# Kernel optimization log

Hardware: AMD Instinct MI355X
Metric: run time of the kernel (lower is better)

Reference implementation:

```python
import jax, jax.numpy as jnp
import numpy as np

K = 3
STRIDE = 1
PAD = 1


def _conv2d(x, w, b):
    y = jax.lax.conv_general_dilated(
        x, w, window_strides=(STRIDE, STRIDE),
        padding=[(PAD, PAD), (PAD, PAD)],
        dimension_numbers=("NCHW", "OIHW", "NCHW"))
    return y + b[None, :, None, None]


def _bilinear_sample(xb, py, px):
    # xb: [C, H, W]; py, px: [K2, Ho, Wo] float sample coords
    C, H, W = xb.shape
    y0 = jnp.floor(py)
    x0 = jnp.floor(px)
    ay = py - y0  # frac weights
    ax = px - x0
    out = jnp.zeros((C,) + py.shape, dtype=xb.dtype)
    corners = [
        (y0, x0, (1.0 - ay) * (1.0 - ax)),
        (y0, x0 + 1.0, (1.0 - ay) * ax),
        (y0 + 1.0, x0, ay * (1.0 - ax)),
        (y0 + 1.0, x0 + 1.0, ay * ax),
    ]
    for yc, xc, wgt in corners:
        valid = (yc >= 0) & (yc < H) & (xc >= 0) & (xc < W)
        yi = jnp.clip(yc, 0, H - 1).astype(jnp.int32)
        xi = jnp.clip(xc, 0, W - 1).astype(jnp.int32)
        g = xb[:, yi, xi]  # [C, K2, Ho, Wo]
        out = out + g * (wgt * valid.astype(xb.dtype))[None]
    return out


def _deform_forward(x, weight, bias, p_weight, p_bias):
    B, Cin, H, W = x.shape
    Cout = weight.shape[0]
    K2 = K * K
    # offset / mask prediction conv
    pout = _conv2d(x, p_weight, p_bias)  # [B, 3*K2, Ho, Wo]
    o1, o2, m = jnp.split(pout, 3, axis=1)
    offset = jnp.concatenate([o1, o2], axis=1)  # [B, 2*K2, Ho, Wo]
    mask = jax.nn.sigmoid(m)  # [B, K2, Ho, Wo]
    Ho, Wo = mask.shape[2], mask.shape[3]
    # torchvision layout: channel 2k = dy_k, 2k+1 = dx_k
    off = offset.reshape(B, K2, 2, Ho, Wo)
    dy, dx = off[:, :, 0], off[:, :, 1]  # [B, K2, Ho, Wo]
    ki = (jnp.arange(K2) // K).astype(x.dtype)  # kernel row
    kj = (jnp.arange(K2) % K).astype(x.dtype)   # kernel col
    base_y = jnp.arange(Ho, dtype=x.dtype) * STRIDE - PAD  # [Ho]
    base_x = jnp.arange(Wo, dtype=x.dtype) * STRIDE - PAD  # [Wo]
    py = base_y[None, None, :, None] + ki[None, :, None, None] + dy
    px = base_x[None, None, None, :] + kj[None, :, None, None] + dx
    sampled = jax.vmap(_bilinear_sample)(x, py, px)  # [B, Cin, K2, Ho, Wo]
    sampled = sampled * mask[:, None]
    w = weight.reshape(Cout, Cin, K2)
    out = jnp.einsum('bckhw,ock->bohw', sampled, w) + bias[None, :, None, None]
    return out


def setup_inputs() -> dict:
    key = jax.random.key(0)
    k1, k2, k3 = jax.random.split(key, 3)
    B, Cin, Cout, H, W = 4, 256, 256, 64, 64
    x = jax.random.normal(k1, (B, Cin, H, W), dtype=jnp.float32)
    fan_in = Cin * K * K
    weight = jax.random.normal(k2, (Cout, Cin, K, K), dtype=jnp.float32) / np.sqrt(fan_in)
    bias = jnp.zeros((Cout,), dtype=jnp.float32)
    # small random offset/mask predictor (zero-init in the original; randomized
    # here so the deformable sampling path is exercised)
    p_weight = jax.random.normal(k3, (3 * K * K, Cin, K, K), dtype=jnp.float32) * 0.02
    p_bias = jnp.zeros((3 * K * K,), dtype=jnp.float32)
    return {"x": x, "weight": weight, "bias": bias, "p_weight": p_weight, "p_bias": p_bias}


def reference(x, weight, bias, p_weight, p_bias):
    return _deform_forward(x, weight, bias, p_weight, p_bias)
```

## Files before the change

kernel.cpp:

```cpp
#include <hip/hip_runtime.h>
#include <stdint.h>


#define CIN 256
#define COUT 256
#define HWS 4096
#define MTOT 16384
#define KTOT 2304
#define SPLITK 8

typedef __attribute__((ext_vector_type(8))) short bf16x8;
typedef __attribute__((ext_vector_type(4))) float f32x4;

__device__ __forceinline__ unsigned short f2bf(float f) {
  unsigned int u = __float_as_uint(f);
  unsigned int r = (u + 0x7fffu + ((u >> 16) & 1u)) >> 16;
  return (unsigned short)r;
}
__device__ __forceinline__ float bf2f(unsigned short u) {
  return __uint_as_float(((unsigned int)u) << 16);
}

__device__ __forceinline__ void gload_lds16(const void* g, void* l) {
  __builtin_amdgcn_global_load_lds((const __attribute__((address_space(1))) void*)g,
                                   (__attribute__((address_space(3))) void*)l, 16, 0, 0);
}

__global__ __launch_bounds__(256) void prep_and_transpose(const float* __restrict__ x,
                                                          const float* __restrict__ w,
                                                          const float* __restrict__ pw,
                                                          unsigned short* __restrict__ xt,
                                                          unsigned short* __restrict__ WB,
                                                          unsigned short* __restrict__ PWs,
                                                          unsigned short* __restrict__ zerop) {
  __shared__ float tile[32][33];
  int bid = blockIdx.x;
  if (bid < 4096) {
    int b = bid >> 10;
    int rest = bid & 1023;
    int hw0 = (rest & 127) * 32;
    int c0 = ((rest >> 7) & 7) * 32;
    int tx = threadIdx.x & 31, ty = threadIdx.x >> 5;
    for (int i = ty; i < 32; i += 8)
      tile[i][tx] = x[(size_t)(b * CIN + c0 + i) * HWS + hw0 + tx];
    __syncthreads();
    for (int r = ty; r < 32; r += 8)
      xt[(size_t)(b * HWS + hw0 + r) * CIN + c0 + tx] = f2bf(tile[tx][r]);
  } else {
    int idx = (bid - 4096) * 256 + threadIdx.x;
    if (idx < 512)
      *(uint4*)(zerop + idx * 8) = make_uint4(0, 0, 0, 0);
    if (idx < KTOT * COUT) {
      int f = idx;
      int e = f & 7;
      int row = (f >> 3) & 15;
      int quad = (f >> 7) & 3;
      int j = (f >> 9) & 15;
      int t = f >> 13;
      int kk = t * 32 + quad * 8 + e;
      int o = j * 16 + row;
      int k = kk >> 8, c = kk & 255;
      WB[f] = f2bf(w[o * KTOT + c * 9 + k]);
    } else {
      int f2 = idx - KTOT * COUT;
      int t_ = f2 & 7;
      int rest = f2 >> 3;
      int j = rest & 31;
      int kk = (rest >> 5) * 8 + t_;
      int k = kk >> 8, c = kk & 255;
      float v = (j < 27) ? pw[j * KTOT + c * 9 + k] : 0.0f;
      PWs[f2] = f2bf(v);
    }
  }
}

__global__ __launch_bounds__(256) void offset_conv_sk(const unsigned short* __restrict__ xt,
                                                      const unsigned short* __restrict__ PWs,
                                                      const unsigned short* __restrict__ zerop,
                                                      float* __restrict__ Pbuf) {
  __shared__ unsigned short Al[64 * 32];
  __shared__ unsigned short Bl[1024];
  int tid = threadIdx.x;
  int lane = tid & 63, wv = tid >> 6;
  int mt = (blockIdx.x & 7) * 32 + (blockIdx.x >> 3);
  int m0 = mt * 64;
  int s = blockIdx.y;
  int b = m0 >> 12;
  int hw0 = m0 & 4095;
  f32x4 acc[2] = {};

  for (int tt = 0; tt < 72 / SPLITK; ++tt) {
    int t = s * (72 / SPLITK) + tt;
    int k = t >> 3, c0 = (t & 7) * 32;
    int dyk = k / 3 - 1;
    int dxk = k % 3 - 1;
    __syncthreads();
    if (tid < 128)
      gload_lds16(PWs + (size_t)t * 1024 + tid * 8, &Bl[tid * 8]);
    {
      int r = tid >> 2;
      int hw = hw0 + r;
      int h = hw >> 6, wwp = hw & 63;
      int y = h + dyk, xx = wwp + dxk;
      bool valid = ((unsigned)y < 64u) && ((unsigned)xx < 64u);
      const unsigned short* src = valid
          ? xt + ((size_t)((b << 12) + (y << 6) + xx) << 8) + c0 + (tid & 3) * 8
          : zerop;
      gload_lds16(src, &Al[tid * 8]);
    }
    __syncthreads();
    int row = lane & 15, quad = lane >> 4;
    bf16x8 af = *(const bf16x8*)&Al[(wv * 16 + row) * 32 + quad * 8];
    for (int j = 0; j < 2; ++j) {
      bf16x8 bfr = *(const bf16x8*)&Bl[(quad * 32 + j * 16 + row) * 8];
      acc[j] = __builtin_amdgcn_mfma_f32_16x16x32_bf16(af, bfr, acc[j], 0, 0, 0);
    }
  }

  int row = lane & 15, quad = lane >> 4;
  for (int j = 0; j < 2; ++j) {
    int n = j * 16 + row;
    for (int r_ = 0; r_ < 4; ++r_) {
      int m = m0 + wv * 16 + quad * 4 + r_;
      Pbuf[((size_t)s * MTOT + m) * 32 + n] = acc[j][r_];
    }
  }
}

__global__ __launch_bounds__(256) void index_prep(const float* __restrict__ Pbuf,
                                                  const float* __restrict__ p_bias,
                                                  int4* __restrict__ DIW) {
  int gid = blockIdx.x * 256 + threadIdx.x;
  int m = gid / 9;
  int k = gid - m * 9;

  float dy = p_bias[2 * k];
  float dx = p_bias[2 * k + 1];
  float mv = p_bias[18 + k];
#pragma unroll
  for (int s = 0; s < SPLITK; ++s) {
    const float* p = Pbuf + ((size_t)s * MTOT + m) * 32;
    dy += p[2 * k];
    dx += p[2 * k + 1];
    mv += p[18 + k];
  }
  float mk = 1.0f / (1.0f + __expf(-mv));

  int hw = m & 4095, h = hw >> 6, ww = hw & 63;
  float py = (float)(h - 1 + k / 3) + dy;
  float px = (float)(ww - 1 + k % 3) + dx;
  float y0f = floorf(py), x0f = floorf(px);
  float ay = py - y0f, ax = px - x0f;
  int y0 = (int)y0f, x0 = (int)x0f;

  float w00 = (1.f - ay) * (1.f - ax) * mk;
  float w01 = (1.f - ay) * ax * mk;
  float w10 = ay * (1.f - ax) * mk;
  float w11 = ay * ax * mk;

  float vy0 = ((unsigned)y0 < 64u) ? 1.f : 0.f;
  float vy1 = ((unsigned)(y0 + 1) < 64u) ? 1.f : 0.f;
  float vx0 = ((unsigned)x0 < 64u) ? 1.f : 0.f;
  float vx1 = ((unsigned)(x0 + 1) < 64u) ? 1.f : 0.f;
  w00 *= vy0 * vx0; w01 *= vy0 * vx1; w10 *= vy1 * vx0; w11 *= vy1 * vx1;

  int yc0 = min(max(y0, 0), 63), yc1 = min(max(y0 + 1, 0), 63);
  int xc0 = min(max(x0, 0), 63), xc1 = min(max(x0 + 1, 0), 63);

  DIW[(size_t)gid * 2] = make_int4((yc0 * 64 + xc0) * 256, (yc0 * 64 + xc1) * 256,
                                   (yc1 * 64 + xc0) * 256, (yc1 * 64 + xc1) * 256);
  float4 w4 = make_float4(w00, w01, w10, w11);
  ((float4*)DIW)[(size_t)gid * 2 + 1] = w4;
}

__device__ __forceinline__ void bilin8(const bf16x8 g00, const bf16x8 g01,
                                       const bf16x8 g10, const bf16x8 g11,
                                       const float4 w4, unsigned short* dst) {
  bf16x8 o8;
#pragma unroll
  for (int e = 0; e < 8; ++e) {
    float v = w4.x * bf2f((unsigned short)g00[e]) + w4.y * bf2f((unsigned short)g01[e]) +
              w4.z * bf2f((unsigned short)g10[e]) + w4.w * bf2f((unsigned short)g11[e]);
    o8[e] = (short)f2bf(v);
  }
  *(bf16x8*)dst = o8;
}

#define MFMA16(A0, A1, A2_, A3, B0, B1, B2, B3)                                          \
  acc[0][0] = __builtin_amdgcn_mfma_f32_16x16x32_bf16(A0, B0, acc[0][0], 0, 0, 0);       \
  acc[0][1] = __builtin_amdgcn_mfma_f32_16x16x32_bf16(A0, B1, acc[0][1], 0, 0, 0);       \
  acc[0][2] = __builtin_amdgcn_mfma_f32_16x16x32_bf16(A0, B2, acc[0][2], 0, 0, 0);       \
  acc[0][3] = __builtin_amdgcn_mfma_f32_16x16x32_bf16(A0, B3, acc[0][3], 0, 0, 0);       \
  acc[1][0] = __builtin_amdgcn_mfma_f32_16x16x32_bf16(A1, B0, acc[1][0], 0, 0, 0);       \
  acc[1][1] = __builtin_amdgcn_mfma_f32_16x16x32_bf16(A1, B1, acc[1][1], 0, 0, 0);       \
  acc[1][2] = __builtin_amdgcn_mfma_f32_16x16x32_bf16(A1, B2, acc[1][2], 0, 0, 0);       \
  acc[1][3] = __builtin_amdgcn_mfma_f32_16x16x32_bf16(A1, B3, acc[1][3], 0, 0, 0);       \
  acc[2][0] = __builtin_amdgcn_mfma_f32_16x16x32_bf16(A2_, B0, acc[2][0], 0, 0, 0);      \
  acc[2][1] = __builtin_amdgcn_mfma_f32_16x16x32_bf16(A2_, B1, acc[2][1], 0, 0, 0);      \
  acc[2][2] = __builtin_amdgcn_mfma_f32_16x16x32_bf16(A2_, B2, acc[2][2], 0, 0, 0);      \
  acc[2][3] = __builtin_amdgcn_mfma_f32_16x16x32_bf16(A2_, B3, acc[2][3], 0, 0, 0);      \
  acc[3][0] = __builtin_amdgcn_mfma_f32_16x16x32_bf16(A3, B0, acc[3][0], 0, 0, 0);       \
  acc[3][1] = __builtin_amdgcn_mfma_f32_16x16x32_bf16(A3, B1, acc[3][1], 0, 0, 0);       \
  acc[3][2] = __builtin_amdgcn_mfma_f32_16x16x32_bf16(A3, B2, acc[3][2], 0, 0, 0);       \
  acc[3][3] = __builtin_amdgcn_mfma_f32_16x16x32_bf16(A3, B3, acc[3][3], 0, 0, 0);

#define FITER(T, PAR, BC0, BC1, BC2, BC3, BN0, BN1, BN2, BN3)                            \
  {                                                                                      \
    if ((T) <= 69) {                                                                     \
      if ((((T) + 2) & 7) == 0) dI4 = Tbl[r][((T) + 2) >> 3][0];                         \
      int cq = (((T) + 2) & 7) * 32 + qo;                                                \
      g00 = *(const bf16x8*)(xtb + dI4.x + cq);                                          \
      g01 = *(const bf16x8*)(xtb + dI4.y + cq);                                          \
      g10 = *(const bf16x8*)(xtb + dI4.z + cq);                                          \
      g11 = *(const bf16x8*)(xtb + dI4.w + cq);                                          \
    }                                                                                    \
    if ((T) <= 70) {                                                                     \
      const unsigned short* bt_ = bpb + (size_t)((T) + 1) * 8192;                        \
      BN0 = *(const bf16x8*)(bt_);                                                       \
      BN1 = *(const bf16x8*)(bt_ + 512);                                                 \
      BN2 = *(const bf16x8*)(bt_ + 1024);                                                \
      BN3 = *(const bf16x8*)(bt_ + 1536);                                                \
    }                                                                                    \
    afr0 = *(const bf16x8*)&As[PAR][row][quad * 8];                                      \
    afr1 = *(const bf16x8*)&As[PAR][16 + row][quad * 8];                                 \
    afr2 = *(const bf16x8*)&As[PAR][32 + row][quad * 8];                                 \
    afr3 = *(const bf16x8*)&As[PAR][48 + row][quad * 8];                                 \
    if ((T) <= 70) {                                                                     \
      if ((((T) + 1) & 7) == 0) dW4 = *(float4*)&Tbl[r][((T) + 1) >> 3][1];              \
      bilin8(gp0, gp1, gp2, gp3, dW4, &As[PAR ^ 1][r][qo]);                              \
    }                                                                                    \
    MFMA16(afr0, afr1, afr2, afr3, BC0, BC1, BC2, BC3)                                   \
    __syncthreads();                                                                     \
  }

__global__ __launch_bounds__(256, 1) void fused_gemm(const unsigned short* __restrict__ xt,
                                                     const int4* __restrict__ DIW,
                                                     const unsigned short* __restrict__ WB,
                                                     const float* __restrict__ bias,
                                                     float* __restrict__ out) {
  __shared__ unsigned short As[2][64][40];
  __shared__ int4 Tbl[64][9][2];

  int tid = threadIdx.x;
  int lane = tid & 63, wv = tid >> 6;
  int mt = (blockIdx.x & 7) * 32 + (blockIdx.x >> 3);
  int mb = mt * 64;
  int b = mb >> 12;
  int hw0 = mb & 4095;
  const unsigned short* xtb = xt + ((size_t)b << 20);

  {
    const int4* src = DIW + (size_t)mb * 18;
    int4* dst = (int4*)Tbl;
    for (int i = tid; i < 1152; i += 256)
      gload_lds16(src + i, dst + i);
  }
  __syncthreads();

  int r = tid >> 2;
  int qo = (tid & 3) * 8;

  int4 dI4 = Tbl[r][0][0];
  float4 dW4 = *(float4*)&Tbl[r][0][1];

  int row = lane & 15, quad = lane >> 4;
  const unsigned short* bpb = WB + (size_t)wv * 4 * 512 + quad * 128 + row * 8;

  f32x4 acc[4][4] = {};
  bf16x8 g00, g01, g10, g11;
  bf16x8 gp0, gp1, gp2, gp3;
  bf16x8 bA0, bA1, bA2, bA3, bB0, bB1, bB2, bB3;
  bf16x8 afr0, afr1, afr2, afr3;

  {
    g00 = *(const bf16x8*)(xtb + dI4.x + qo);
    g01 = *(const bf16x8*)(xtb + dI4.y + qo);
    g10 = *(const bf16x8*)(xtb + dI4.z + qo);
    g11 = *(const bf16x8*)(xtb + dI4.w + qo);
    bA0 = *(const bf16x8*)(bpb);
    bA1 = *(const bf16x8*)(bpb + 512);
    bA2 = *(const bf16x8*)(bpb + 1024);
    bA3 = *(const bf16x8*)(bpb + 1536);
    bilin8(g00, g01, g10, g11, dW4, &As[0][r][qo]);
    g00 = *(const bf16x8*)(xtb + dI4.x + 32 + qo);
    g01 = *(const bf16x8*)(xtb + dI4.y + 32 + qo);
    g10 = *(const bf16x8*)(xtb + dI4.z + 32 + qo);
    g11 = *(const bf16x8*)(xtb + dI4.w + 32 + qo);
  }
  __syncthreads();

#pragma unroll 1
  for (int t = 0; t < 72; t += 2) {
    gp0 = g00; gp1 = g01; gp2 = g10; gp3 = g11;
    FITER(t, 0, bA0, bA1, bA2, bA3, bB0, bB1, bB2, bB3)
    gp0 = g00; gp1 = g01; gp2 = g10; gp3 = g11;
    FITER(t + 1, 1, bB0, bB1, bB2, bB3, bA0, bA1, bA2, bA3)
  }

#pragma unroll
  for (int j = 0; j < 4; ++j) {
    int o = wv * 64 + j * 16 + row;
    float bo = bias[o];
#pragma unroll
    for (int i = 0; i < 4; ++i) {
      int hw = hw0 + i * 16 + quad * 4;
      float4 v;
      v.x = acc[i][j][0] + bo;
      v.y = acc[i][j][1] + bo;
      v.z = acc[i][j][2] + bo;
      v.w = acc[i][j][3] + bo;
      *(float4*)(out + (((size_t)(b * COUT + o)) << 12) + hw) = v;
    }
  }
}

extern "C" void kernel_launch(void* const* d_in, const int* in_sizes, int n_in,
                              void* d_out, int out_size, void* d_ws, size_t ws_size,
                              hipStream_t stream) {
  const float* x        = (const float*)d_in[0];
  const float* weight   = (const float*)d_in[1];
  const float* bias     = (const float*)d_in[2];
  const float* p_weight = (const float*)d_in[3];
  const float* p_bias   = (const float*)d_in[4];
  float* out = (float*)d_out;
  char* ws = (char*)d_ws;

  const size_t OFF_XT   = 0;
  const size_t OFF_WB   = OFF_XT + 8388608;
  const size_t OFF_PW   = OFF_WB + 1179648;
  const size_t OFF_P    = OFF_PW + 147456;
  const size_t OFF_ZP   = OFF_P + 16777216;
  const size_t OFF_DIW  = OFF_ZP + 8192;

  unsigned short* xt    = (unsigned short*)(ws + OFF_XT);
  unsigned short* WB    = (unsigned short*)(ws + OFF_WB);
  unsigned short* PWs   = (unsigned short*)(ws + OFF_PW);
  float* Pbuf           = (float*)(ws + OFF_P);
  unsigned short* zerop = (unsigned short*)(ws + OFF_ZP);
  int4* DIW             = (int4*)(ws + OFF_DIW);

  prep_and_transpose<<<4096 + 2592, 256, 0, stream>>>(x, weight, p_weight, xt, WB, PWs, zerop);
  offset_conv_sk<<<dim3(MTOT / 64, SPLITK), 256, 0, stream>>>(xt, PWs, zerop, Pbuf);
  index_prep<<<576, 256, 0, stream>>>(Pbuf, p_bias, DIW);
  fused_gemm<<<256, 256, 0, stream>>>(xt, DIW, WB, bias, out);
}
```

Baseline: 141.9 us.

## Double threads per block in fused deformable GEMM, halving per-thread work

The fused gather+GEMM kernel now launches 512 threads per block instead of 256. Each of the eight waves covers 32 output channels instead of 64, and each thread bilinearly samples 4 channels instead of 8. This lowers register pressure and per-thread latency, so more waves are available to hide gather and MFMA latency. In exchange, the grid is still only 256 blocks, each thread issues narrower 8-byte gather loads, and barrier cost rises with the larger block.

```diff
diff --git a/kernel.cpp b/kernel.cpp
--- a/kernel.cpp
+++ b/kernel.cpp
@@ -20,6 +20,8 @@
 __device__ __forceinline__ float bf2f(unsigned short u) {
   return __uint_as_float(((unsigned int)u) << 16);
 }
+__device__ __forceinline__ float bflo(unsigned int u) { return __uint_as_float(u << 16); }
+__device__ __forceinline__ float bfhi(unsigned int u) { return __uint_as_float(u & 0xffff0000u); }
 
 __device__ __forceinline__ void gload_lds16(const void* g, void* l) {
   __builtin_amdgcn_global_load_lds((const __attribute__((address_space(1))) void*)g,
@@ -173,53 +175,42 @@
   ((float4*)DIW)[(size_t)gid * 2 + 1] = w4;
 }
 
-__device__ __forceinline__ void bilin8(const bf16x8 g00, const bf16x8 g01,
-                                       const bf16x8 g10, const bf16x8 g11,
-                                       const float4 w4, unsigned short* dst) {
-  bf16x8 o8;
-#pragma unroll
-  for (int e = 0; e < 8; ++e) {
-    float v = w4.x * bf2f((unsigned short)g00[e]) + w4.y * bf2f((unsigned short)g01[e]) +
-              w4.z * bf2f((unsigned short)g10[e]) + w4.w * bf2f((unsigned short)g11[e]);
-    o8[e] = (short)f2bf(v);
-  }
-  *(bf16x8*)dst = o8;
-}
-
-#define MFMA16(A0, A1, A2_, A3, B0, B1, B2, B3)                                          \
+__device__ __forceinline__ void bilin4p(const uint2 c00, const uint2 c01,
+                                        const uint2 c10, const uint2 c11,
+                                        const float4 w4, unsigned short* dst) {
+  float v0 = w4.x * bflo(c00.x) + w4.y * bflo(c01.x) + w4.z * bflo(c10.x) + w4.w * bflo(c11.x);
+  float v1 = w4.x * bfhi(c00.x) + w4.y * bfhi(c01.x) + w4.z * bfhi(c10.x) + w4.w * bfhi(c11.x);
+  float v2 = w4.x * bflo(c00.y) + w4.y * bflo(c01.y) + w4.z * bflo(c10.y) + w4.w * bflo(c11.y);
+  float v3 = w4.x * bfhi(c00.y) + w4.y * bfhi(c01.y) + w4.z * bfhi(c10.y) + w4.w * bfhi(c11.y);
+  ushort4 o;
+  o.x = f2bf(v0); o.y = f2bf(v1); o.z = f2bf(v2); o.w = f2bf(v3);
+  *(ushort4*)dst = o;
+}
+
+#define MFMA8(A0, A1, A2_, A3, B0, B1)                                                   \
   acc[0][0] = __builtin_amdgcn_mfma_f32_16x16x32_bf16(A0, B0, acc[0][0], 0, 0, 0);       \
   acc[0][1] = __builtin_amdgcn_mfma_f32_16x16x32_bf16(A0, B1, acc[0][1], 0, 0, 0);       \
-  acc[0][2] = __builtin_amdgcn_mfma_f32_16x16x32_bf16(A0, B2, acc[0][2], 0, 0, 0);       \
-  acc[0][3] = __builtin_amdgcn_mfma_f32_16x16x32_bf16(A0, B3, acc[0][3], 0, 0, 0);       \
   acc[1][0] = __builtin_amdgcn_mfma_f32_16x16x32_bf16(A1, B0, acc[1][0], 0, 0, 0);       \
   acc[1][1] = __builtin_amdgcn_mfma_f32_16x16x32_bf16(A1, B1, acc[1][1], 0, 0, 0);       \
-  acc[1][2] = __builtin_amdgcn_mfma_f32_16x16x32_bf16(A1, B2, acc[1][2], 0, 0, 0);       \
-  acc[1][3] = __builtin_amdgcn_mfma_f32_16x16x32_bf16(A1, B3, acc[1][3], 0, 0, 0);       \
   acc[2][0] = __builtin_amdgcn_mfma_f32_16x16x32_bf16(A2_, B0, acc[2][0], 0, 0, 0);      \
   acc[2][1] = __builtin_amdgcn_mfma_f32_16x16x32_bf16(A2_, B1, acc[2][1], 0, 0, 0);      \
-  acc[2][2] = __builtin_amdgcn_mfma_f32_16x16x32_bf16(A2_, B2, acc[2][2], 0, 0, 0);      \
-  acc[2][3] = __builtin_amdgcn_mfma_f32_16x16x32_bf16(A2_, B3, acc[2][3], 0, 0, 0);      \
   acc[3][0] = __builtin_amdgcn_mfma_f32_16x16x32_bf16(A3, B0, acc[3][0], 0, 0, 0);       \
-  acc[3][1] = __builtin_amdgcn_mfma_f32_16x16x32_bf16(A3, B1, acc[3][1], 0, 0, 0);       \
-  acc[3][2] = __builtin_amdgcn_mfma_f32_16x16x32_bf16(A3, B2, acc[3][2], 0, 0, 0);       \
-  acc[3][3] = __builtin_amdgcn_mfma_f32_16x16x32_bf16(A3, B3, acc[3][3], 0, 0, 0);
-
-#define FITER(T, PAR, BC0, BC1, BC2, BC3, BN0, BN1, BN2, BN3)                            \
+  acc[3][1] = __builtin_amdgcn_mfma_f32_16x16x32_bf16(A3, B1, acc[3][1], 0, 0, 0);
+
+#define FITER(T, PAR, BC0, BC1, BN0, BN1)                                                \
   {                                                                                      \
     if ((T) <= 69) {                                                                     \
       if ((((T) + 2) & 7) == 0) dI4 = Tbl[r][((T) + 2) >> 3][0];                         \
       int cq = (((T) + 2) & 7) * 32 + qo;                                                \
-      g00 = *(const bf16x8*)(xtb + dI4.x + cq);                                          \
-      g01 = *(const bf16x8*)(xtb + dI4.y + cq);                                          \
-      g10 = *(const bf16x8*)(xtb + dI4.z + cq);                                          \
-      g11 = *(const bf16x8*)(xtb + dI4.w + cq);                                          \
+      g00 = *(const uint2*)(xtb + dI4.x + cq);                                           \
+      g01 = *(const uint2*)(xtb + dI4.y + cq);                                           \
+      g10 = *(const uint2*)(xtb + dI4.z + cq);                                           \
+      g11 = *(const uint2*)(xtb + dI4.w + cq);                                           \
     }                                                                                    \
     if ((T) <= 70) {                                                                     \
       const unsigned short* bt_ = bpb + (size_t)((T) + 1) * 8192;                        \
       BN0 = *(const bf16x8*)(bt_);                                                       \
       BN1 = *(const bf16x8*)(bt_ + 512);                                                 \
-      BN2 = *(const bf16x8*)(bt_ + 1024);                                                \
-      BN3 = *(const bf16x8*)(bt_ + 1536);                                                \
     }                                                                                    \
     afr0 = *(const bf16x8*)&As[PAR][row][quad * 8];                                      \
     afr1 = *(const bf16x8*)&As[PAR][16 + row][quad * 8];                                 \
@@ -227,13 +218,13 @@
     afr3 = *(const bf16x8*)&As[PAR][48 + row][quad * 8];                                 \
     if ((T) <= 70) {                                                                     \
       if ((((T) + 1) & 7) == 0) dW4 = *(float4*)&Tbl[r][((T) + 1) >> 3][1];              \
-      bilin8(gp0, gp1, gp2, gp3, dW4, &As[PAR ^ 1][r][qo]);                              \
+      bilin4p(gp0, gp1, gp2, gp3, dW4, &As[PAR ^ 1][r][qo]);                             \
     }                                                                                    \
-    MFMA16(afr0, afr1, afr2, afr3, BC0, BC1, BC2, BC3)                                   \
+    MFMA8(afr0, afr1, afr2, afr3, BC0, BC1)                                              \
     __syncthreads();                                                                     \
   }
 
-__global__ __launch_bounds__(256, 1) void fused_gemm(const unsigned short* __restrict__ xt,
+__global__ __launch_bounds__(512, 2) void fused_gemm(const unsigned short* __restrict__ xt,
                                                      const int4* __restrict__ DIW,
                                                      const unsigned short* __restrict__ WB,
                                                      const float* __restrict__ bias,
@@ -252,54 +243,52 @@
   {
     const int4* src = DIW + (size_t)mb * 18;
     int4* dst = (int4*)Tbl;
-    for (int i = tid; i < 1152; i += 256)
+    for (int i = tid; i < 1152; i += 512)
       gload_lds16(src + i, dst + i);
   }
   __syncthreads();
 
-  int r = tid >> 2;
-  int qo = (tid & 3) * 8;
+  int r = tid >> 3;
+  int qo = (tid & 7) * 4;
 
   int4 dI4 = Tbl[r][0][0];
   float4 dW4 = *(float4*)&Tbl[r][0][1];
 
   int row = lane & 15, quad = lane >> 4;
-  const unsigned short* bpb = WB + (size_t)wv * 4 * 512 + quad * 128 + row * 8;
-
-  f32x4 acc[4][4] = {};
-  bf16x8 g00, g01, g10, g11;
-  bf16x8 gp0, gp1, gp2, gp3;
-  bf16x8 bA0, bA1, bA2, bA3, bB0, bB1, bB2, bB3;
+  const unsigned short* bpb = WB + (size_t)(wv * 2) * 512 + quad * 128 + row * 8;
+
+  f32x4 acc[4][2] = {};
+  uint2 g00, g01, g10, g11;
+  uint2 gp0, gp1, gp2, gp3;
+  bf16x8 bA0, bA1, bB0, bB1;
   bf16x8 afr0, afr1, afr2, afr3;
 
   {
-    g00 = *(const bf16x8*)(xtb + dI4.x + qo);
-    g01 = *(const bf16x8*)(xtb + dI4.y + qo);
-    g10 = *(const bf16x8*)(xtb + dI4.z + qo);
-    g11 = *(const bf16x8*)(xtb + dI4.w + qo);
+    g00 = *(const uint2*)(xtb + dI4.x + qo);
+    g01 = *(const uint2*)(xtb + dI4.y + qo);
+    g10 = *(const uint2*)(xtb + dI4.z + qo);
+    g11 = *(const uint2*)(xtb + dI4.w + qo);
     bA0 = *(const bf16x8*)(bpb);
     bA1 = *(const bf16x8*)(bpb + 512);
-    bA2 = *(const bf16x8*)(bpb + 1024);
-    bA3 = *(const bf16x8*)(bpb + 1536);
-    bilin8(g00, g01, g10, g11, dW4, &As[0][r][qo]);
-    g00 = *(const bf16x8*)(xtb + dI4.x + 32 + qo);
-    g01 = *(const bf16x8*)(xtb + dI4.y + 32 + qo);
-    g10 = *(const bf16x8*)(xtb + dI4.z + 32 + qo);
-    g11 = *(const bf16x8*)(xtb + dI4.w + 32 + qo);
+    bilin4p(g00, g01, g10, g11, dW4, &As[0][r][qo]);
+    g00 = *(const uint2*)(xtb + dI4.x + 32 + qo);
+    g01 = *(const uint2*)(xtb + dI4.y + 32 + qo);
+    g10 = *(const uint2*)(xtb + dI4.z + 32 + qo);
+    g11 = *(const uint2*)(xtb + dI4.w + 32 + qo);
   }
   __syncthreads();
 
 #pragma unroll 1
   for (int t = 0; t < 72; t += 2) {
     gp0 = g00; gp1 = g01; gp2 = g10; gp3 = g11;
-    FITER(t, 0, bA0, bA1, bA2, bA3, bB0, bB1, bB2, bB3)
+    FITER(t, 0, bA0, bA1, bB0, bB1)
     gp0 = g00; gp1 = g01; gp2 = g10; gp3 = g11;
-    FITER(t + 1, 1, bB0, bB1, bB2, bB3, bA0, bA1, bA2, bA3)
+    FITER(t + 1, 1, bB0, bB1, bA0, bA1)
   }
 
 #pragma unroll
-  for (int j = 0; j < 4; ++j) {
-    int o = wv * 64 + j * 16 + row;
+  for (int j = 0; j < 2; ++j) {
+    int o = wv * 32 + j * 16 + row;
     float bo = bias[o];
 #pragma unroll
     for (int i = 0; i < 4; ++i) {
@@ -342,5 +331,5 @@
   prep_and_transpose<<<4096 + 2592, 256, 0, stream>>>(x, weight, p_weight, xt, WB, PWs, zerop);
   offset_conv_sk<<<dim3(MTOT / 64, SPLITK), 256, 0, stream>>>(xt, PWs, zerop, Pbuf);
   index_prep<<<576, 256, 0, stream>>>(Pbuf, p_bias, DIW);
-  fused_gemm<<<256, 256, 0, stream>>>(xt, DIW, WB, bias, out);
-}
+  fused_gemm<<<256, 512, 0, stream>>>(xt, DIW, WB, bias, out);
+}
```

Measured after the change: 150.6 us. 1.06x slower.
